# Kernel tuning notes

Measured on AMD Instinct MI355X. Metric: run time of the kernel, lower is better.

## Reference

```python
import jax, jax.numpy as jnp
import numpy as np

D = 1024
H = 16
B = 4
L = 1024
EPS = 1e-5


def _ln(x, g, b):
    m = jnp.mean(x, axis=-1, keepdims=True)
    v = jnp.mean((x - m) ** 2, axis=-1, keepdims=True)
    return (x - m) / jnp.sqrt(v + EPS) * g + b


def _bn_eval(x, g, b, mean, var):
    # x: [B, L, C]; per-channel batchnorm in eval mode
    return (x - mean) / jnp.sqrt(var + EPS) * g + b


def setup_inputs() -> dict:
    key = jax.random.key(0)
    ks = jax.random.split(key, 16)
    s = 0.02
    return {
        "q": jax.random.normal(ks[0], (B, L, D), jnp.float32),
        "wq": jax.random.normal(ks[1], (D, D), jnp.float32) * s,
        "bq": jax.random.normal(ks[2], (D,), jnp.float32) * s,
        "wk": jax.random.normal(ks[3], (D, D), jnp.float32) * s,
        "bk": jax.random.normal(ks[4], (D,), jnp.float32) * s,
        "wv": jax.random.normal(ks[5], (D, D), jnp.float32) * s,
        "bv": jax.random.normal(ks[6], (D,), jnp.float32) * s,
        "wo": jax.random.normal(ks[7], (D, D), jnp.float32) * s,
        "bo": jax.random.normal(ks[8], (D,), jnp.float32) * s,
        "w1": jax.random.normal(ks[9], (4 * D, D), jnp.float32) * s,
        "bn1_g": jax.random.uniform(ks[10], (4 * D,), jnp.float32, 0.5, 1.5),
        "bn1_b": jax.random.normal(ks[11], (4 * D,), jnp.float32) * s,
        "bn1_m": jax.random.normal(ks[12], (4 * D,), jnp.float32) * s,
        "bn1_v": jax.random.uniform(ks[13], (4 * D,), jnp.float32, 0.5, 1.5),
        "w2": jax.random.normal(ks[14], (D, 4 * D), jnp.float32) * s,
        "bn2_g": jax.random.uniform(ks[15], (D,), jnp.float32, 0.5, 1.5),
        "bn2_b": jnp.zeros((D,), jnp.float32),
        "bn2_m": jnp.zeros((D,), jnp.float32),
        "bn2_v": jnp.ones((D,), jnp.float32),
        "ln1_g": jnp.ones((D,), jnp.float32),
        "ln1_b": jnp.zeros((D,), jnp.float32),
        "ln3_g": jnp.ones((D,), jnp.float32),
        "ln3_b": jnp.zeros((D,), jnp.float32),
    }


def reference(q, wq, bq, wk, bk, wv, bv, wo, bo,
              w1, bn1_g, bn1_b, bn1_m, bn1_v,
              w2, bn2_g, bn2_b, bn2_m, bn2_v,
              ln1_g, ln1_b, ln3_g, ln3_b):
    hd = D // H
    scale = hd ** -0.5
    # conv1x1 projections == per-token linear: [B,L,D] @ [D,D]^T + bias
    qp = (q @ wq.T + bq).reshape(B, L, H, hd)
    kp = (q @ wk.T + bk).reshape(B, L, H, hd)
    vp = (q @ wv.T + bv).reshape(B, L, H, hd)
    attn = jnp.einsum('blhd,bmhd->bhlm', qp, kp) * scale  # [B,H,L,L]
    attn = jax.nn.softmax(attn, axis=-1)
    out = jnp.einsum('bhlm,bmhd->blhd', attn, vp).reshape(B, L, D)
    out = out @ wo.T + bo
    # post-norm residual block (norm_first=False, use_residual=True)
    x = _ln(q + out, ln1_g, ln1_b)
    # conv-MLP: 1x1 conv -> BN(eval) -> GELU(exact) -> 1x1 conv -> BN(eval)
    h = x @ w1.T                                   # [B,L,4D]
    h = jax.nn.gelu(_bn_eval(h, bn1_g, bn1_b, bn1_m, bn1_v), approximate=False)
    h = _bn_eval(h @ w2.T, bn2_g, bn2_b, bn2_m, bn2_v)  # [B,L,D]
    x = _ln(x + h, ln3_g, ln3_b)
    return x
```

## Files before the change

kernel.cpp:

```cpp
#include <hip/hip_runtime.h>
#include <math.h>

#define EPS 1e-5f

typedef unsigned short ushort_t;
typedef __attribute__((ext_vector_type(8))) __bf16 bf16x8;
typedef __attribute__((ext_vector_type(4))) __bf16 bf16x4;
typedef __attribute__((ext_vector_type(4))) float f32x4;

#define MFMA16(a, b, c) __builtin_amdgcn_mfma_f32_16x16x32_bf16(a, b, c, 0, 0, 0)

#define QSCALE2 0.18033688011112042f

__device__ __forceinline__ unsigned short f2bf(float f) {
  unsigned u = __float_as_uint(f);
  u += 0x7fffu + ((u >> 16) & 1u);
  return (unsigned short)(u >> 16);
}

__device__ __forceinline__ void gload16(const void* g, void* l) {
  __builtin_amdgcn_global_load_lds(
      (__attribute__((address_space(1))) void*)(g),
      (__attribute__((address_space(3))) void*)(l), 16, 0, 0);
}

__global__ __launch_bounds__(256) void cast_all_k(
    const float* __restrict__ wq, const float* __restrict__ wk,
    const float* __restrict__ wv, const float* __restrict__ wo,
    const float* __restrict__ w1, const float* __restrict__ w2,
    const float* __restrict__ q, ushort_t* __restrict__ wqkv,
    ushort_t* __restrict__ wob, ushort_t* __restrict__ w1b,
    ushort_t* __restrict__ w2b, ushort_t* __restrict__ qbf) {
  const int b = blockIdx.x;
  const float* src;
  ushort_t* dst;
  int idx;
  if (b < 2048) {
    const int s = b >> 9;
    src = (s == 0) ? wq : (s == 1) ? wk : (s == 2) ? wv : wo;
    dst = (s == 3) ? wob : wqkv + s * 1048576;
    idx = (b & 511) * 2048 + threadIdx.x * 8;
  } else if (b < 4096) {
    src = w1; dst = w1b; idx = (b - 2048) * 2048 + threadIdx.x * 8;
  } else if (b < 6144) {
    src = w2; dst = w2b; idx = (b - 4096) * 2048 + threadIdx.x * 8;
  } else {
    src = q; dst = qbf; idx = (b - 6144) * 2048 + threadIdx.x * 8;
  }
  float4 a = *(const float4*)(src + idx);
  float4 c = *(const float4*)(src + idx + 4);
  uint4 u;
  u.x = (unsigned)f2bf(a.x) | ((unsigned)f2bf(a.y) << 16);
  u.y = (unsigned)f2bf(a.z) | ((unsigned)f2bf(a.w) << 16);
  u.z = (unsigned)f2bf(c.x) | ((unsigned)f2bf(c.y) << 16);
  u.w = (unsigned)f2bf(c.z) | ((unsigned)f2bf(c.w) << 16);
  *(uint4*)(dst + idx) = u;
}

__global__ __launch_bounds__(256) void bnparam_k(
    const float* __restrict__ g1, const float* __restrict__ b1,
    const float* __restrict__ m1, const float* __restrict__ v1,
    const float* __restrict__ g2, const float* __restrict__ b2,
    const float* __restrict__ m2, const float* __restrict__ v2,
    float* __restrict__ sc1, float* __restrict__ sh1,
    float* __restrict__ sc2, float* __restrict__ sh2) {
  int i = blockIdx.x * 256 + threadIdx.x;
  if (i < 4096) {
    float s = g1[i] * rsqrtf(v1[i] + EPS);
    sc1[i] = s;
    sh1[i] = b1[i] - m1[i] * s;
  } else if (i < 5120) {
    int j = i - 4096;
    float s = g2[j] * rsqrtf(v2[j] + EPS);
    sc2[j] = s;
    sh2[j] = b2[j] - m2[j] * s;
  }
}

template <int KDIM, int EPI, int TM, int TN, int WM, int WN, int NTHR, int GX, int GY>
__global__ __launch_bounds__(NTHR, 2) void gemm_bt(const ushort_t* __restrict__ A,
                                                   const ushort_t* __restrict__ W,
                                                   const float* __restrict__ p0,
                                                   const float* __restrict__ p1,
                                                   const float* __restrict__ p2,
                                                   float* __restrict__ outF,
                                                   ushort_t* __restrict__ outB) {
  constexpr int BM = 16 * TM * WM, BN = 16 * TN * WN;
  constexpr int LDS_STAGE = 2 * (BM + BN) * 128;
  constexpr int LDS_TR = (EPI == 0) ? 128 * 136 * 2 : 0;
  __shared__ alignas(16) char pool[(LDS_STAGE > LDS_TR) ? LDS_STAGE : LDS_TR];
  constexpr int LA = BM * 8 / NTHR;
  constexpr int LB = BN * 8 / NTHR;

  constexpr int NWG = GX * GY;
  const int id = blockIdx.x;
  const int pos = (id & 7) * (NWG / 8) + (id >> 3);
  const int grp = pos / (8 * GX);
  const int rem = pos % (8 * GX);
  const int by = grp * 8 + (rem & 7);
  const int bx = rem >> 3;
  const int bm = by * BM, bn = bx * BN;

  const int tid = threadIdx.x;
  const int lane = tid & 63;
  const int wid = tid >> 6;
  const int wr = wid / WN, wc = wid % WN;
  const int fr = lane & 15;
  const int kg = lane >> 4;

  const char* Ag0 = (const char*)(A + (size_t)bm * KDIM);
  const char* Bg0 = (const char*)(W + (size_t)bn * KDIM);

#define STAGE(bufi, t_)                                                        \
  do {                                                                         \
    const char* Ag = Ag0 + (size_t)(t_)*128;                                   \
    const char* Bg = Bg0 + (size_t)(t_)*128;                                   \
    char* Ab = pool + (bufi) * (BM * 128);                                     \
    char* Bb = pool + 2 * BM * 128 + (bufi) * (BN * 128);                      \
    _Pragma("unroll") for (int li = 0; li < LA; ++li) {                        \
      const int f = li * NTHR + tid;                                           \
      const int row = f >> 3;                                                  \
      const int gl = (f & 7) ^ (row & 7);                                      \
      gload16(Ag + (size_t)row * (KDIM * 2) + gl * 16,                         \
              Ab + (li * NTHR + wid * 64) * 16);                               \
    }                                                                          \
    _Pragma("unroll") for (int li = 0; li < LB; ++li) {                        \
      const int f = li * NTHR + tid;                                           \
      const int row = f >> 3;                                                  \
      const int gl = (f & 7) ^ (row & 7);                                      \
      gload16(Bg + (size_t)row * (KDIM * 2) + gl * 16,                         \
              Bb + (li * NTHR + wid * 64) * 16);                               \
    }                                                                          \
  } while (0)

  f32x4 acc[TM][TN];
#pragma unroll
  for (int i = 0; i < TM; ++i)
#pragma unroll
    for (int j = 0; j < TN; ++j)
#pragma unroll
      for (int r = 0; r < 4; ++r) acc[i][j][r] = 0.f;

  STAGE(0, 0);
  asm volatile("s_waitcnt vmcnt(0)" ::: "memory");
  __builtin_amdgcn_s_barrier();

  constexpr int NT = KDIM / 64;
  for (int t = 0; t < NT; ++t) {
    const int b = t & 1;
    if (t + 1 < NT) STAGE(b ^ 1, t + 1);
    const char* Ac = pool + b * (BM * 128);
    const char* Bc = pool + 2 * BM * 128 + b * (BN * 128);
#pragma unroll
    for (int s = 0; s < 2; ++s) {
      bf16x8 bfv[TN];
#pragma unroll
      for (int nf = 0; nf < TN; ++nf) {
        const int row = wc * (16 * TN) + nf * 16 + fr;
        bfv[nf] = *(const bf16x8*)(Bc + row * 128 + (((s * 4 + kg) ^ (row & 7)) * 16));
      }
#pragma unroll
      for (int mf = 0; mf < TM; ++mf) {
        const int row = wr * (16 * TM) + mf * 16 + fr;
        bf16x8 af = *(const bf16x8*)(Ac + row * 128 + (((s * 4 + kg) ^ (row & 7)) * 16));
#pragma unroll
        for (int nf = 0; nf < TN; ++nf) acc[mf][nf] = MFMA16(af, bfv[nf], acc[mf][nf]);
      }
    }
    asm volatile("s_waitcnt vmcnt(0)" ::: "memory");
    __builtin_amdgcn_s_barrier();
  }
#undef STAGE

  if constexpr (EPI == 0) {
    if (bn < 2048) {
#pragma unroll
      for (int mf = 0; mf < TM; ++mf) {
#pragma unroll
        for (int nf = 0; nf < TN; ++nf) {
#pragma unroll
          for (int r = 0; r < 4; ++r) {
            const int m = bm + wr * (16 * TM) + mf * 16 + kg * 4 + r;
            const int n = bn + wc * (16 * TN) + nf * 16 + fr;
            const int sel = n >> 10;
            const int nl = n & 1023;
            float v = acc[mf][nf][r] + ((sel == 0) ? p0[nl] : p1[nl]);
            if (sel == 0) v *= QSCALE2;
            const int b_ = m >> 10, tok = m & 1023;
            const int h_ = nl >> 6, d_ = nl & 63;
            outB[(size_t)sel * 4194304 + (((size_t)(b_ * 16 + h_) * 1024 + tok) * 64 + d_)] =
                f2bf(v);
          }
        }
      }
    } else {
      __syncthreads();
      ushort_t* T = (ushort_t*)pool;
#pragma unroll
      for (int mf = 0; mf < TM; ++mf) {
#pragma unroll
        for (int nf = 0; nf < TN; ++nf) {
          const int ml = wr * (16 * TM) + mf * 16 + kg * 4;
          const int nl = wc * (16 * TN) + nf * 16 + fr;
          const float bias = p2[(bn & 1023) + nl];
          bf16x4 pw;
#pragma unroll
          for (int r = 0; r < 4; ++r) pw[r] = (__bf16)(acc[mf][nf][r] + bias);
          *(bf16x4*)(T + nl * 136 + ml) = pw;
        }
      }
      __syncthreads();
      const int b_ = bm >> 10;
      const int tokb = bm & 1023;
#pragma unroll
      for (int it = 0; it < 8; ++it) {
        const int g = it * 256 + tid;
        const int nl = g >> 4;
        const int m0 = (g & 15) * 8;
        bf16x8 v = *(const bf16x8*)(T + nl * 136 + m0);
        const int nloc = (bn - 2048) + nl;
        const int h_ = nloc >> 6, d_ = nloc & 63;
        *(bf16x8*)(outB + 8388608 + (((size_t)(b_ * 16 + h_) * 64 + d_) << 10) + tokb + m0) = v;
      }
    }
  } else {
#pragma unroll
    for (int mf = 0; mf < TM; ++mf) {
#pragma unroll
      for (int nf = 0; nf < TN; ++nf) {
#pragma unroll
        for (int r = 0; r < 4; ++r) {
          const int m = bm + wr * (16 * TM) + mf * 16 + kg * 4 + r;
          const int n = bn + wc * (16 * TN) + nf * 16 + fr;
          float v = acc[mf][nf][r];
          if constexpr (EPI == 1) {
            v += p0[n] + p1[(size_t)m * 1024 + n];
            outF[(size_t)m * 1024 + n] = v;
          } else if constexpr (EPI == 2) {
            float tt = v * p0[n] + p1[n];
            float u = tt * (0.7978845608f + 0.0356774081f * tt * tt);
            float e = exp2f(u * 2.8853900818f);
            float ge = tt * (1.f - 1.f / (e + 1.f));
            outB[(size_t)m * 4096 + n] = f2bf(ge);
          } else {
            outF[(size_t)m * 1024 + n] = v * p0[n] + p1[n];
          }
        }
      }
    }
  }
}

template <int KDIM, int TM, int TN, int GX, int GY>
__global__ __launch_bounds__(256, 2) void gemm3s(const ushort_t* __restrict__ A,
                                                 const ushort_t* __restrict__ W,
                                                 const float* __restrict__ sc,
                                                 const float* __restrict__ sh,
                                                 float* __restrict__ outF) {
  constexpr int BM = 32 * TM, BN = 32 * TN;
  __shared__ alignas(16) char pool[3 * (BM + BN) * 128];
  constexpr int LA = BM * 8 / 256;
  constexpr int LB = BN * 8 / 256;

  constexpr int NWG = GX * GY;
  const int id = blockIdx.x;
  const int pos = (id & 7) * (NWG / 8) + (id >> 3);
  const int grp = pos / (8 * GX);
  const int rem = pos % (8 * GX);
  const int by = grp * 8 + (rem & 7);
  const int bx = rem >> 3;
  const int bm = by * BM, bn = bx * BN;

  const int tid = threadIdx.x;
  const int lane = tid & 63;
  const int wid = tid >> 6;
  const int wr = wid >> 1, wc = wid & 1;
  const int fr = lane & 15;
  const int kg = lane >> 4;

  const char* Ag0 = (const char*)(A + (size_t)bm * KDIM);
  const char* Bg0 = (const char*)(W + (size_t)bn * KDIM);

#define STAGE3(bufi, t_)                                                       \
  do {                                                                         \
    const char* Ag = Ag0 + (size_t)(t_)*128;                                   \
    const char* Bg = Bg0 + (size_t)(t_)*128;                                   \
    char* Ab = pool + (bufi) * (BM * 128);                                     \
    char* Bb = pool + 3 * BM * 128 + (bufi) * (BN * 128);                      \
    _Pragma("unroll") for (int li = 0; li < LA; ++li) {                        \
      const int f = li * 256 + tid;                                            \
      const int row = f >> 3;                                                  \
      const int gl = (f & 7) ^ (row & 7);                                      \
      gload16(Ag + (size_t)row * (KDIM * 2) + gl * 16,                         \
              Ab + (li * 256 + wid * 64) * 16);                                \
    }                                                                          \
    _Pragma("unroll") for (int li = 0; li < LB; ++li) {                        \
      const int f = li * 256 + tid;                                            \
      const int row = f >> 3;                                                  \
      const int gl = (f & 7) ^ (row & 7);                                      \
      gload16(Bg + (size_t)row * (KDIM * 2) + gl * 16,                         \
              Bb + (li * 256 + wid * 64) * 16);                                \
    }                                                                          \
  } while (0)

  f32x4 acc[TM][TN];
#pragma unroll
  for (int i = 0; i < TM; ++i)
#pragma unroll
    for (int j = 0; j < TN; ++j)
#pragma unroll
      for (int r = 0; r < 4; ++r) acc[i][j][r] = 0.f;

  STAGE3(0, 0);
  STAGE3(1, 1);
  asm volatile("s_waitcnt vmcnt(6)" ::: "memory");
  __builtin_amdgcn_s_barrier();

  constexpr int NT = KDIM / 64;
  int cb = 0;
  for (int t = 0; t < NT; ++t) {
    if (t + 2 < NT) {
      const int nb = (cb + 2 >= 3) ? cb - 1 : cb + 2;
      STAGE3(nb, t + 2);
    }
    const char* Ac = pool + cb * (BM * 128);
    const char* Bc = pool + 3 * BM * 128 + cb * (BN * 128);
#pragma unroll
    for (int s = 0; s < 2; ++s) {
      bf16x8 bfv[TN];
#pragma unroll
      for (int nf = 0; nf < TN; ++nf) {
        const int row = wc * (16 * TN) + nf * 16 + fr;
        bfv[nf] = *(const bf16x8*)(Bc + row * 128 + (((s * 4 + kg) ^ (row & 7)) * 16));
      }
#pragma unroll
      for (int mf = 0; mf < TM; ++mf) {
        const int row = wr * (16 * TM) + mf * 16 + fr;
        bf16x8 af = *(const bf16x8*)(Ac + row * 128 + (((s * 4 + kg) ^ (row & 7)) * 16));
#pragma unroll
        for (int nf = 0; nf < TN; ++nf) acc[mf][nf] = MFMA16(af, bfv[nf], acc[mf][nf]);
      }
    }
    if (t + 2 < NT)
      asm volatile("s_waitcnt vmcnt(6)" ::: "memory");
    else
      asm volatile("s_waitcnt vmcnt(0)" ::: "memory");
    asm volatile("s_waitcnt lgkmcnt(0)" ::: "memory");
    __builtin_amdgcn_s_barrier();
    cb = (cb + 1 >= 3) ? 0 : cb + 1;
  }
#undef STAGE3

#pragma unroll
  for (int mf = 0; mf < TM; ++mf) {
#pragma unroll
    for (int nf = 0; nf < TN; ++nf) {
      const int n = bn + wc * (16 * TN) + nf * 16 + fr;
      const float scn = sc[n], shn = sh[n];
#pragma unroll
      for (int r = 0; r < 4; ++r) {
        const int m = bm + wr * (16 * TM) + mf * 16 + kg * 4 + r;
        outF[(size_t)m * 1024 + n] = acc[mf][nf][r] * scn + shn;
      }
    }
  }
}

__global__ __launch_bounds__(512) void attn_k(const ushort_t* __restrict__ qp,
                                              const ushort_t* __restrict__ kp,
                                              const ushort_t* __restrict__ vt,
                                              ushort_t* __restrict__ aout) {
  __shared__ ushort_t Kt[2][4096];
  __shared__ ushort_t Vt[2][4096];
  __shared__ ushort_t P[8][16][72];
  const int tid = threadIdx.x;
  const int lane = tid & 63;
  const int wid = tid >> 6;
  const int fr = lane & 15;
  const int kg = lane >> 4;
  const int id = blockIdx.x;
  const int slot = id >> 3;
  const int bh = ((id & 7) << 3) | (slot >> 3);
  const int qc = slot & 7;
  const int b_ = bh >> 4, h_ = bh & 15;

  const size_t base = (size_t)bh << 10;
  const int qrow = qc * 128 + wid * 16 + fr;
  bf16x8 qf0 = *(const bf16x8*)(qp + ((base + qrow) << 6) + kg * 8);
  bf16x8 qf1 = *(const bf16x8*)(qp + ((base + qrow) << 6) + 32 + kg * 8);

  const int srow = tid >> 3;
  const int sg16 = ((tid & 7) ^ (srow & 7)) * 16;
  const char* kTileB = (const char*)kp + ((size_t)bh << 17);
  const char* vTileB = (const char*)vt + ((size_t)bh << 17);
  const size_t koff = (size_t)srow * 128 + sg16;
  const size_t voff = (size_t)srow * 2048 + sg16;

#define STAGE(bufi, kt_)                                                      \
  do {                                                                        \
    gload16(kTileB + (size_t)(kt_)*8192 + koff, (char*)Kt[bufi] + wid * 1024); \
    gload16(vTileB + (size_t)(kt_)*128 + voff, (char*)Vt[bufi] + wid * 1024);  \
  } while (0)

  f32x4 oacc[4];
#pragma unroll
  for (int d = 0; d < 4; ++d)
#pragma unroll
    for (int r = 0; r < 4; ++r) oacc[d][r] = 0.f;
  float mrun = -3.0e38f, lrun = 0.f;

  STAGE(0, 0);
  __syncthreads();

  for (int kt = 0; kt < 16; ++kt) {
    const int c = kt & 1;
    if (kt < 15) STAGE(c ^ 1, kt + 1);
    const char* Kc = (const char*)Kt[c];
    const char* Vc = (const char*)Vt[c];

    f32x4 sacc[4];
#pragma unroll
    for (int nf = 0; nf < 4; ++nf)
#pragma unroll
      for (int r = 0; r < 4; ++r) sacc[nf][r] = 0.f;
    __builtin_amdgcn_s_setprio(1);
#pragma unroll
    for (int nf = 0; nf < 4; ++nf) {
      const int r_ = nf * 16 + fr;
      const char* kr = Kc + r_ * 128;
      bf16x8 kf0 = *(const bf16x8*)(kr + ((kg ^ (r_ & 7)) * 16));
      bf16x8 kf1 = *(const bf16x8*)(kr + (((kg + 4) ^ (r_ & 7)) * 16));
      sacc[nf] = MFMA16(kf0, qf0, sacc[nf]);
      sacc[nf] = MFMA16(kf1, qf1, sacc[nf]);
    }
    __builtin_amdgcn_s_setprio(0);
    float mx = sacc[0][0];
#pragma unroll
    for (int nf = 0; nf < 4; ++nf)
#pragma unroll
      for (int r = 0; r < 4; ++r) mx = fmaxf(mx, sacc[nf][r]);
    mx = fmaxf(mx, __shfl_xor(mx, 16));
    mx = fmaxf(mx, __shfl_xor(mx, 32));
    const float mn = fmaxf(mrun, mx);
    const float c_ = exp2f(mrun - mn);
    float rs = 0.f;
#pragma unroll
    for (int nf = 0; nf < 4; ++nf) {
      bf16x4 pw;
#pragma unroll
      for (int r = 0; r < 4; ++r) {
        float ev = exp2f(sacc[nf][r] - mn);
        rs += ev;
        pw[r] = (__bf16)ev;
      }
      *(bf16x4*)(&P[wid][fr][nf * 16 + kg * 4]) = pw;
    }
    rs += __shfl_xor(rs, 16);
    rs += __shfl_xor(rs, 32);
    lrun = lrun * c_ + rs;
    mrun = mn;
    float cb[4];
#pragma unroll
    for (int r = 0; r < 4; ++r) cb[r] = __shfl(c_, kg * 4 + r);
#pragma unroll
    for (int d = 0; d < 4; ++d)
#pragma unroll
      for (int r = 0; r < 4; ++r) oacc[d][r] *= cb[r];
    bf16x8 pa0 = *(const bf16x8*)(&P[wid][fr][kg * 8]);
    bf16x8 pa1 = *(const bf16x8*)(&P[wid][fr][32 + kg * 8]);
    __builtin_amdgcn_s_setprio(1);
#pragma unroll
    for (int df = 0; df < 4; ++df) {
      const int r_ = df * 16 + fr;
      const char* vr_ = Vc + r_ * 128;
      bf16x8 vf0 = *(const bf16x8*)(vr_ + ((kg ^ (r_ & 7)) * 16));
      bf16x8 vf1 = *(const bf16x8*)(vr_ + (((kg + 4) ^ (r_ & 7)) * 16));
      oacc[df] = MFMA16(pa0, vf0, oacc[df]);
      oacc[df] = MFMA16(pa1, vf1, oacc[df]);
    }
    __builtin_amdgcn_s_setprio(0);
    __syncthreads();
  }
#undef STAGE

  float linv[4];
#pragma unroll
  for (int r = 0; r < 4; ++r) linv[r] = 1.f / __shfl(lrun, kg * 4 + r);
#pragma unroll
  for (int df = 0; df < 4; ++df) {
#pragma unroll
    for (int r = 0; r < 4; ++r) {
      const int tok = qc * 128 + wid * 16 + kg * 4 + r;
      const int d_ = df * 16 + fr;
      aout[((size_t)(b_ * 1024 + tok) * 16 + h_) * 64 + d_] = f2bf(oacc[df][r] * linv[r]);
    }
  }
}

template <int MODE>
__global__ __launch_bounds__(256) void ln_k(const float* __restrict__ in1,
                                            const float* __restrict__ in2,
                                            const float* __restrict__ g,
                                            const float* __restrict__ bt,
                                            float* __restrict__ outF,
                                            ushort_t* __restrict__ outB) {
  const int row = blockIdx.x;
  const int tid = threadIdx.x;
  const size_t off = (size_t)row * 1024 + tid * 4;
  float4 v = *(const float4*)(in1 + off);
  if (MODE == 1) {
    float4 u = *(const float4*)(in2 + off);
    v.x += u.x; v.y += u.y; v.z += u.z; v.w += u.w;
  }
  float s = v.x + v.y + v.z + v.w;
  float q = v.x * v.x + v.y * v.y + v.z * v.z + v.w * v.w;
#pragma unroll
  for (int o = 32; o > 0; o >>= 1) {
    s += __shfl_down(s, o);
    q += __shfl_down(q, o);
  }
  __shared__ float rs[4], rq[4], stat[2];
  const int wid = tid >> 6, lane = tid & 63;
  if (lane == 0) { rs[wid] = s; rq[wid] = q; }
  __syncthreads();
  if (tid == 0) {
    float S = rs[0] + rs[1] + rs[2] + rs[3];
    float Q = rq[0] + rq[1] + rq[2] + rq[3];
    float mean = S * (1.f / 1024.f);
    float var = Q * (1.f / 1024.f) - mean * mean;
    stat[0] = mean;
    stat[1] = rsqrtf(var + EPS);
  }
  __syncthreads();
  const float mean = stat[0], rstd = stat[1];
  const int c = tid * 4;
  float4 o4;
  o4.x = (v.x - mean) * rstd * g[c] + bt[c];
  o4.y = (v.y - mean) * rstd * g[c + 1] + bt[c + 1];
  o4.z = (v.z - mean) * rstd * g[c + 2] + bt[c + 2];
  o4.w = (v.w - mean) * rstd * g[c + 3] + bt[c + 3];
  *(float4*)(outF + off) = o4;
  if (MODE == 0) {
    ushort4 ub;
    ub.x = f2bf(o4.x); ub.y = f2bf(o4.y); ub.z = f2bf(o4.z); ub.w = f2bf(o4.w);
    *(ushort4*)(outB + off) = ub;
  }
}

extern "C" void kernel_launch(void* const* d_in, const int* in_sizes, int n_in,
                              void* d_out, int out_size, void* d_ws, size_t ws_size,
                              hipStream_t stream) {
  const float* q    = (const float*)d_in[0];
  const float* wq   = (const float*)d_in[1];
  const float* bq   = (const float*)d_in[2];
  const float* wk   = (const float*)d_in[3];
  const float* bk   = (const float*)d_in[4];
  const float* wv   = (const float*)d_in[5];
  const float* bv   = (const float*)d_in[6];
  const float* wo   = (const float*)d_in[7];
  const float* bo   = (const float*)d_in[8];
  const float* w1   = (const float*)d_in[9];
  const float* bn1g = (const float*)d_in[10];
  const float* bn1b = (const float*)d_in[11];
  const float* bn1m = (const float*)d_in[12];
  const float* bn1v = (const float*)d_in[13];
  const float* w2   = (const float*)d_in[14];
  const float* bn2g = (const float*)d_in[15];
  const float* bn2b = (const float*)d_in[16];
  const float* bn2m = (const float*)d_in[17];
  const float* bn2v = (const float*)d_in[18];
  const float* ln1g = (const float*)d_in[19];
  const float* ln1b = (const float*)d_in[20];
  const float* ln3g = (const float*)d_in[21];
  const float* ln3b = (const float*)d_in[22];

  char* ws = (char*)d_ws;
  const size_t MB = 1u << 20;
  ushort_t* wqkv = (ushort_t*)(ws);
  ushort_t* w1b  = (ushort_t*)(ws + 6 * MB);
  ushort_t* w2b  = (ushort_t*)(ws + 14 * MB);
  ushort_t* wob  = (ushort_t*)(ws + 22 * MB);
  float* sc1 = (float*)(ws + 24 * MB);
  float* sh1 = sc1 + 4096;
  float* sc2 = sh1 + 4096;
  float* sh2 = sc2 + 1024;
  ushort_t* qbf  = (ushort_t*)(ws + 25 * MB);
  ushort_t* qp   = (ushort_t*)(ws + 33 * MB);
  ushort_t* aout = (ushort_t*)(ws + 57 * MB);
  ushort_t* xbf  = (ushort_t*)(ws + 65 * MB);
  float*    h2   = (float*)(ws + 73 * MB);
  ushort_t* h1   = (ushort_t*)(ws + 33 * MB);
  float* X = (float*)d_out;

  const int NM = 1024 * 1024;
  cast_all_k<<<8192, 256, 0, stream>>>(wq, wk, wv, wo, w1, w2, q, wqkv, wob, w1b, w2b, qbf);
  bnparam_k<<<20, 256, 0, stream>>>(bn1g, bn1b, bn1m, bn1v, bn2g, bn2b, bn2m, bn2v,
                                    sc1, sh1, sc2, sh2);

  gemm_bt<1024, 0, 4, 4, 2, 2, 256, 24, 32><<<768, 256, 0, stream>>>(
      qbf, wqkv, bq, bk, bv, nullptr, qp);
  attn_k<<<512, 512, 0, stream>>>(qp, qp + 4 * NM, qp + 8 * NM, aout);
  gemm_bt<1024, 1, 4, 2, 2, 2, 256, 16, 32><<<512, 256, 0, stream>>>(
      aout, wob, bo, q, nullptr, X, nullptr);
  ln_k<0><<<4096, 256, 0, stream>>>(X, nullptr, ln1g, ln1b, X, xbf);
  gemm_bt<1024, 2, 8, 4, 2, 4, 512, 16, 16><<<256, 512, 0, stream>>>(
      xbf, w1b, sc1, sh1, nullptr, nullptr, h1);
  gemm3s<4096, 4, 2, 16, 32><<<512, 256, 0, stream>>>(h1, w2b, sc2, sh2, h2);
  ln_k<1><<<4096, 256, 0, stream>>>(X, h2, ln3g, ln3b, X, nullptr);
}
```

Before: 209.9 us.

## Add pipelined FFN1 GEMM kernel and lazy softmax rescaling in attention

Replaces the FFN1 GEMM (with fused BN+GELU epilogue) with a new kernel. It uses 256x128 tiles, a 3-stage LDS ring filled by global_load_lds, and load issue interleaved between MFMA phases with explicit barriers and waitcnts. Separately, the attention online softmax now skips the rescale of the output accumulator and running sum when the new block max does not exceed the running max by more than a threshold. That cuts exp and multiply work per block, at the risk of larger unnormalized exponent values in bf16/fp32.

Measured after the change: 220.0 us. +4.8%, slower.

```diff
diff --git a/kernel.cpp b/kernel.cpp
--- a/kernel.cpp
+++ b/kernel.cpp
@@ -236,16 +236,142 @@
           if constexpr (EPI == 1) {
             v += p0[n] + p1[(size_t)m * 1024 + n];
             outF[(size_t)m * 1024 + n] = v;
-          } else if constexpr (EPI == 2) {
-            float tt = v * p0[n] + p1[n];
-            float u = tt * (0.7978845608f + 0.0356774081f * tt * tt);
-            float e = exp2f(u * 2.8853900818f);
-            float ge = tt * (1.f - 1.f / (e + 1.f));
-            outB[(size_t)m * 4096 + n] = f2bf(ge);
           } else {
             outF[(size_t)m * 1024 + n] = v * p0[n] + p1[n];
           }
         }
+      }
+    }
+  }
+}
+
+template <int KDIM, int GX, int GY>
+__global__ __launch_bounds__(512, 1) void gemm_fi(const ushort_t* __restrict__ A,
+                                                  const ushort_t* __restrict__ W,
+                                                  const float* __restrict__ sc,
+                                                  const float* __restrict__ sh,
+                                                  ushort_t* __restrict__ outB) {
+  __shared__ alignas(16) char pool[3 * 49152];
+
+  constexpr int NWG = GX * GY;
+  const int id = blockIdx.x;
+  const int pos = (id & 7) * (NWG / 8) + (id >> 3);
+  const int grp = pos / (8 * GX);
+  const int rem = pos % (8 * GX);
+  const int by = grp * 8 + (rem & 7);
+  const int bx = rem >> 3;
+  const int bm = by * 256, bn = bx * 128;
+
+  const int tid = threadIdx.x;
+  const int lane = tid & 63;
+  const int wid = tid >> 6;
+  const int wr = wid >> 2;
+  const int wc = wid & 3;
+  const int fr = lane & 15;
+  const int kg = lane >> 4;
+
+  const char* Ag0 = (const char*)(A + (size_t)bm * KDIM);
+  const char* Bg0 = (const char*)(W + (size_t)bn * KDIM);
+
+#define FI_A(j, t_, li)                                                        \
+  do {                                                                         \
+    const int f = (li)*512 + tid;                                              \
+    const int row = f >> 3;                                                    \
+    const int gl = (f & 7) ^ (row & 7);                                        \
+    gload16(Ag0 + (size_t)row * (KDIM * 2) + (size_t)(t_)*128 + gl * 16,       \
+            pool + (j)*49152 + ((li)*512 + wid * 64) * 16);                    \
+  } while (0)
+#define FI_B(j, t_, li)                                                        \
+  do {                                                                         \
+    const int f = (li)*512 + tid;                                              \
+    const int row = f >> 3;                                                    \
+    const int gl = (f & 7) ^ (row & 7);                                        \
+    gload16(Bg0 + (size_t)row * (KDIM * 2) + (size_t)(t_)*128 + gl * 16,       \
+            pool + (j)*49152 + 32768 + ((li)*512 + wid * 64) * 16);            \
+  } while (0)
+#define FI_LDA(mh, s)                                                          \
+  _Pragma("unroll") for (int mf2 = 0; mf2 < 4; ++mf2) {                        \
+    const int row = wr * 128 + (mh)*64 + mf2 * 16 + fr;                        \
+    af[mf2] = *(const bf16x8*)(Ac + row * 128 + ((((s)*4 + kg) ^ (row & 7)) * 16)); \
+  }
+#define FI_LDB(s)                                                              \
+  _Pragma("unroll") for (int nf = 0; nf < 2; ++nf) {                           \
+    const int row = wc * 32 + nf * 16 + fr;                                    \
+    bfv[nf] = *(const bf16x8*)(Bc + row * 128 + ((((s)*4 + kg) ^ (row & 7)) * 16)); \
+  }
+#define FI_MFMA(mh)                                                            \
+  __builtin_amdgcn_s_setprio(1);                                               \
+  _Pragma("unroll") for (int mf2 = 0; mf2 < 4; ++mf2)                          \
+  _Pragma("unroll") for (int nf = 0; nf < 2; ++nf)                             \
+      acc[(mh)*4 + mf2][nf] = MFMA16(af[mf2], bfv[nf], acc[(mh)*4 + mf2][nf]); \
+  __builtin_amdgcn_s_setprio(0);
+#define FI_BAR __builtin_amdgcn_s_barrier()
+#define FI_LGK asm volatile("s_waitcnt lgkmcnt(0)" ::: "memory")
+
+  f32x4 acc[8][2];
+#pragma unroll
+  for (int i = 0; i < 8; ++i)
+#pragma unroll
+    for (int j = 0; j < 2; ++j)
+#pragma unroll
+      for (int r = 0; r < 4; ++r) acc[i][j][r] = 0.f;
+
+  FI_A(0, 0, 0); FI_A(0, 0, 1); FI_A(0, 0, 2); FI_A(0, 0, 3);
+  FI_B(0, 0, 0); FI_B(0, 0, 1);
+  FI_A(1, 1, 0); FI_A(1, 1, 1); FI_A(1, 1, 2); FI_A(1, 1, 3);
+  FI_B(1, 1, 0); FI_B(1, 1, 1);
+  asm volatile("s_waitcnt vmcnt(6)" ::: "memory");
+  __builtin_amdgcn_s_barrier();
+
+  constexpr int NT = KDIM / 64;
+  int j = 0, jn = 2;
+  for (int t = 0; t < NT; ++t) {
+    const char* Ac = pool + j * 49152;
+    const char* Bc = pool + j * 49152 + 32768;
+    const bool more = (t + 2 < NT);
+    bf16x8 af[4], bfv[2];
+    FI_LDA(0, 0); FI_LDB(0);
+    if (more) { FI_A(jn, t + 2, 0); FI_A(jn, t + 2, 1); }
+    FI_BAR; FI_LGK; FI_MFMA(0); FI_BAR;
+    FI_LDA(1, 0);
+    if (more) { FI_A(jn, t + 2, 2); FI_A(jn, t + 2, 3); }
+    FI_BAR; FI_LGK; FI_MFMA(1); FI_BAR;
+    FI_LDA(0, 1); FI_LDB(1);
+    if (more) { FI_B(jn, t + 2, 0); }
+    FI_BAR; FI_LGK; FI_MFMA(0); FI_BAR;
+    FI_LDA(1, 1);
+    if (more) {
+      FI_B(jn, t + 2, 1);
+      asm volatile("s_waitcnt vmcnt(6)" ::: "memory");
+    } else {
+      asm volatile("s_waitcnt vmcnt(0)" ::: "memory");
+    }
+    FI_BAR; FI_LGK; FI_MFMA(1); FI_BAR;
+    j = (j + 1 == 3) ? 0 : j + 1;
+    jn = (jn + 1 == 3) ? 0 : jn + 1;
+  }
+#undef FI_A
+#undef FI_B
+#undef FI_LDA
+#undef FI_LDB
+#undef FI_MFMA
+#undef FI_BAR
+#undef FI_LGK
+
+#pragma unroll
+  for (int mf = 0; mf < 8; ++mf) {
+#pragma unroll
+    for (int nf = 0; nf < 2; ++nf) {
+      const int n = bn + wc * 32 + nf * 16 + fr;
+      const float scn = sc[n], shn = sh[n];
+#pragma unroll
+      for (int r = 0; r < 4; ++r) {
+        const int m = bm + wr * 128 + mf * 16 + kg * 4 + r;
+        float tt = acc[mf][nf][r] * scn + shn;
+        float u = tt * (0.7978845608f + 0.0356774081f * tt * tt);
+        float e = exp2f(u * 2.8853900818f);
+        float ge = tt * (1.f - 1.f / (e + 1.f));
+        outB[(size_t)m * 4096 + n] = f2bf(ge);
       }
     }
   }
@@ -441,8 +567,8 @@
       for (int r = 0; r < 4; ++r) mx = fmaxf(mx, sacc[nf][r]);
     mx = fmaxf(mx, __shfl_xor(mx, 16));
     mx = fmaxf(mx, __shfl_xor(mx, 32));
-    const float mn = fmaxf(mrun, mx);
-    const float c_ = exp2f(mrun - mn);
+    const bool skip = __all((mx - mrun) <= 11.5416f);
+    const float mn = skip ? mrun : fmaxf(mrun, mx);
     float rs = 0.f;
 #pragma unroll
     for (int nf = 0; nf < 4; ++nf) {
@@ -457,15 +583,20 @@
     }
     rs += __shfl_xor(rs, 16);
     rs += __shfl_xor(rs, 32);
-    lrun = lrun * c_ + rs;
-    mrun = mn;
-    float cb[4];
-#pragma unroll
-    for (int r = 0; r < 4; ++r) cb[r] = __shfl(c_, kg * 4 + r);
-#pragma unroll
-    for (int d = 0; d < 4; ++d)
-#pragma unroll
-      for (int r = 0; r < 4; ++r) oacc[d][r] *= cb[r];
+    if (skip) {
+      lrun += rs;
+    } else {
+      const float c_ = exp2f(mrun - mn);
+      lrun = lrun * c_ + rs;
+      mrun = mn;
+      float cb[4];
+#pragma unroll
+      for (int r = 0; r < 4; ++r) cb[r] = __shfl(c_, kg * 4 + r);
+#pragma unroll
+      for (int d = 0; d < 4; ++d)
+#pragma unroll
+        for (int r = 0; r < 4; ++r) oacc[d][r] *= cb[r];
+    }
     bf16x8 pa0 = *(const bf16x8*)(&P[wid][fr][kg * 8]);
     bf16x8 pa1 = *(const bf16x8*)(&P[wid][fr][32 + kg * 8]);
     __builtin_amdgcn_s_setprio(1);
@@ -603,8 +734,7 @@
   gemm_bt<1024, 1, 4, 2, 2, 2, 256, 16, 32><<<512, 256, 0, stream>>>(
       aout, wob, bo, q, nullptr, X, nullptr);
   ln_k<0><<<4096, 256, 0, stream>>>(X, nullptr, ln1g, ln1b, X, xbf);
-  gemm_bt<1024, 2, 8, 4, 2, 4, 512, 16, 16><<<256, 512, 0, stream>>>(
-      xbf, w1b, sc1, sh1, nullptr, nullptr, h1);
+  gemm_fi<1024, 32, 16><<<512, 512, 0, stream>>>(xbf, w1b, sc1, sh1, h1);
   gemm3s<4096, 4, 2, 16, 32><<<512, 256, 0, stream>>>(h1, w2b, sc2, sh2, h2);
   ln_k<1><<<4096, 256, 0, stream>>>(X, h2, ln3g, ln3b, X, nullptr);
 }
```
